# Kernel tuning notes

Hardware: AMD Instinct MI355X
Metric: run time of the kernel (lower is better)

Reference implementation:

```python
import jax, jax.numpy as jnp
import numpy as np

N_HEAD = 16
LN_EPS = 1e-5


def _ln(x, w, b):
    # torch LayerNorm computed in float32 then cast back (see LayerNorm.forward)
    xf = x.astype(jnp.float32)
    mu = jnp.mean(xf, axis=-1, keepdims=True)
    var = jnp.mean(jnp.square(xf - mu), axis=-1, keepdims=True)
    return ((xf - mu) * jax.lax.rsqrt(var + LN_EPS) * w + b).astype(x.dtype)


def setup_inputs() -> dict:
    key = jax.random.key(0)
    ks = jax.random.split(key, 16)
    B, S, C = 4, 1500, 1024
    A = 256  # adapter_dim
    F = 4 * C
    s = 0.02
    return {
        "x": jax.random.normal(ks[0], (B, S, C), jnp.float32),
        "Wq": jax.random.normal(ks[1], (C, C), jnp.float32) * s,
        "bq": jnp.zeros((C,), jnp.float32),
        "Wk": jax.random.normal(ks[2], (C, C), jnp.float32) * s,
        "Wv": jax.random.normal(ks[3], (C, C), jnp.float32) * s,
        "bv": jnp.zeros((C,), jnp.float32),
        "Wo": jax.random.normal(ks[4], (C, C), jnp.float32) * s,
        "bo": jnp.zeros((C,), jnp.float32),
        "ln_attn_w": jnp.ones((C,), jnp.float32),
        "ln_attn_b": jnp.zeros((C,), jnp.float32),
        "W1": jax.random.normal(ks[5], (F, C), jnp.float32) * s,
        "b1": jnp.zeros((F,), jnp.float32),
        "W2": jax.random.normal(ks[6], (C, F), jnp.float32) * s,
        "b2": jnp.zeros((C,), jnp.float32),
        "ln_mlp_w": jnp.ones((C,), jnp.float32),
        "ln_mlp_b": jnp.zeros((C,), jnp.float32),
        "Wds": jax.random.normal(ks[7], (A, C), jnp.float32) * s,
        "bds": jnp.zeros((A,), jnp.float32),
        "Wus": jax.random.normal(ks[8], (C, A), jnp.float32) * s,
        "bus": jnp.zeros((C,), jnp.float32),
    }


def reference(x, Wq, bq, Wk, Wv, bv, Wo, bo, ln_attn_w, ln_attn_b,
              W1, b1, W2, b2, ln_mlp_w, ln_mlp_b, Wds, bds, Wus, bus):
    B, S, C = x.shape
    H = N_HEAD
    D = C // H
    scale = D ** -0.25  # applied to both q and k, per qkv_attention

    # --- self-attention ---
    h = _ln(x, ln_attn_w, ln_attn_b)
    q = (h @ Wq.T + bq).reshape(B, S, H, D) * scale
    k = (h @ Wk.T).reshape(B, S, H, D) * scale  # key has no bias
    v = (h @ Wv.T + bv).reshape(B, S, H, D)
    qk = jnp.einsum("bqhd,bkhd->bhqk", q, k).astype(jnp.float32)
    w = jax.nn.softmax(qk, axis=-1).astype(x.dtype)
    wv = jnp.einsum("bhqk,bkhd->bqhd", w, v).reshape(B, S, C)
    x = x + (wv @ Wo.T + bo)

    # --- MLP (exact GELU, as nn.GELU default) ---
    h = _ln(x, ln_mlp_w, ln_mlp_b)
    x = x + (jax.nn.gelu(h @ W1.T + b1, approximate=False) @ W2.T + b2)

    # --- bottleneck adapter: x + us(gelu(ds(x))) ---
    x = x + (jax.nn.gelu(x @ Wds.T + bds, approximate=False) @ Wus.T + bus)
    return x
```

## Files before the change

kernel.cpp:

```cpp
#include <hip/hip_runtime.h>
#include <hip/hip_bf16.h>
#include <math.h>

typedef __bf16 bf16;
typedef __bf16 bf16x8 __attribute__((ext_vector_type(8)));
typedef float  f32x4  __attribute__((ext_vector_type(4)));

__device__ __forceinline__ void load16_lds(const bf16* g, bf16* l) {
    __builtin_amdgcn_global_load_lds(
        (__attribute__((address_space(1))) void*)(g),
        (__attribute__((address_space(3))) void*)(l), 16, 0, 0);
}

__device__ __forceinline__ float gelu_f(float x) {
    float u = 1.5957691216057308f * (x + 0.044715f * x * x * x);
    float e = __expf(u);
    float th = 1.0f - 2.0f / (1.0f + e);
    return 0.5f * x * (1.0f + th);
}

struct ConvArgs {
    const float* src[19];
    bf16* dst[19];
    int n[19];
    int bstart[20];
};
__global__ __launch_bounds__(256) void convert_many(ConvArgs a) {
    int blk = blockIdx.x;
    int s = 0;
    while (blk >= a.bstart[s + 1]) s++;
    const float* src = a.src[s];
    bf16* dst = a.dst[s];
    int n = a.n[s];
    int i0 = (blk - a.bstart[s]) * 2048;
#pragma unroll
    for (int e = 0; e < 8; e++) {
        int i = i0 + threadIdx.x + e * 256;
        if (i < n) dst[i] = (bf16)src[i];
    }
}

__global__ void zero_kernel(bf16* dst, int n) {
    int i = blockIdx.x * blockDim.x + threadIdx.x;
    if (i < n) dst[i] = (bf16)0.0f;
}

template<class XT>
__global__ __launch_bounds__(256) void ln_kernel(
    const XT* __restrict__ X, const bf16* __restrict__ w,
    const bf16* __restrict__ b, bf16* __restrict__ out)
{
    const int C = 1024;
    const int row = blockIdx.x;
    const int tid = threadIdx.x;
    const XT* xr = X + (size_t)row * C;
    float x0 = (float)xr[tid * 4 + 0], x1 = (float)xr[tid * 4 + 1];
    float x2 = (float)xr[tid * 4 + 2], x3 = (float)xr[tid * 4 + 3];
    float s  = x0 + x1 + x2 + x3;
    float sq = x0*x0 + x1*x1 + x2*x2 + x3*x3;
#pragma unroll
    for (int off = 32; off >= 1; off >>= 1) {
        s  += __shfl_xor(s,  off, 64);
        sq += __shfl_xor(sq, off, 64);
    }
    __shared__ float red[8];
    int wave = tid >> 6;
    if ((tid & 63) == 0) { red[wave] = s; red[4 + wave] = sq; }
    __syncthreads();
    float ts = red[0] + red[1] + red[2] + red[3];
    float tq = red[4] + red[5] + red[6] + red[7];
    float mean = ts * (1.0f / C);
    float var  = tq * (1.0f / C) - mean * mean;
    float rstd = rsqrtf(var + 1e-5f);
    float w0 = (float)w[tid*4+0], w1 = (float)w[tid*4+1], w2 = (float)w[tid*4+2], w3 = (float)w[tid*4+3];
    float b0 = (float)b[tid*4+0], b1 = (float)b[tid*4+1], b2 = (float)b[tid*4+2], b3 = (float)b[tid*4+3];
    bf16* orow = out + (size_t)row * C + tid * 4;
    orow[0] = (bf16)((x0 - mean) * rstd * w0 + b0);
    orow[1] = (bf16)((x1 - mean) * rstd * w1 + b1);
    orow[2] = (bf16)((x2 - mean) * rstd * w2 + b2);
    orow[3] = (bf16)((x3 - mean) * rstd * w3 + b3);
}

template<int ACT, int OMODE, class RT, class OT>
__global__ __launch_bounds__(256) void gemm_kernel(
    const bf16* __restrict__ A, const bf16* __restrict__ W,
    const bf16* __restrict__ bias, const RT* __restrict__ resid,
    OT* __restrict__ out, bf16* __restrict__ out_k, bf16* __restrict__ out_v,
    int M, int N, int K, float scale, int gmT, int gnT, int mQ)
{
    const int lin = blockIdx.x;
    const int xcd = lin & 7;
    const int t_  = lin >> 3;
    const int mt_ = (xcd & 3) + 4 * (t_ % mQ);
    const int nt_ = (xcd >> 2) + 2 * (t_ / mQ);
    if (mt_ >= gmT || nt_ >= gnT) return;
    const int m0 = mt_ * 128;
    const int n0 = nt_ * 128;

    __shared__ __align__(16) bf16 As[2][16 * 512];
    __shared__ __align__(16) bf16 Bs[2][16 * 512];
    const int tid = threadIdx.x;
    const int wave = tid >> 6, lane = tid & 63;
    const int lane15 = lane & 15, quad = lane >> 4;
    const int wm0 = (wave >> 1) * 64;
    const int wn0 = (wave & 1) * 64;
    f32x4 acc[4][4] = {};

    int ra0 = m0 + (2 * wave)     * 16 + lane15; if (ra0 > M - 1) ra0 = M - 1;
    int ra1 = m0 + (2 * wave + 1) * 16 + lane15; if (ra1 > M - 1) ra1 = M - 1;
    const int rb0 = n0 + (2 * wave)     * 16 + lane15;
    const int rb1 = n0 + (2 * wave + 1) * 16 + lane15;
    const bf16* a0 = A + (size_t)ra0 * K + quad * 8;
    const bf16* a1 = A + (size_t)ra1 * K + quad * 8;
    const bf16* w0 = W + (size_t)rb0 * K + quad * 8;
    const bf16* w1 = W + (size_t)rb1 * K + quad * 8;

    auto stage = [&](int buf, int k0) {
#pragma unroll
        for (int kk = 0; kk < 2; kk++) {
            load16_lds(a0 + k0 + kk * 32, &As[buf][((2 * wave)     * 2 + kk) * 512]);
            load16_lds(a1 + k0 + kk * 32, &As[buf][((2 * wave + 1) * 2 + kk) * 512]);
            load16_lds(w0 + k0 + kk * 32, &Bs[buf][((2 * wave)     * 2 + kk) * 512]);
            load16_lds(w1 + k0 + kk * 32, &Bs[buf][((2 * wave + 1) * 2 + kk) * 512]);
        }
    };

    stage(0, 0);
    asm volatile("s_waitcnt vmcnt(0)" ::: "memory");
    __builtin_amdgcn_s_barrier();
    __builtin_amdgcn_sched_barrier(0);

    const int nsteps = K >> 6;
    int cur = 0;
    for (int t = 0; t < nsteps; t++) {
        if (t + 1 < nsteps) stage(cur ^ 1, (t + 1) << 6);
#pragma unroll
        for (int kk = 0; kk < 2; kk++) {
            bf16x8 af[4], bfr[4];
#pragma unroll
            for (int tt = 0; tt < 4; tt++) {
                af[tt]  = *(const bf16x8*)(&As[cur][(((wm0 >> 4) + tt) * 2 + kk) * 512 + lane * 8]);
                bfr[tt] = *(const bf16x8*)(&Bs[cur][(((wn0 >> 4) + tt) * 2 + kk) * 512 + lane * 8]);
            }
#pragma unroll
            for (int mt = 0; mt < 4; mt++)
#pragma unroll
                for (int nt = 0; nt < 4; nt++)
                    acc[mt][nt] = __builtin_amdgcn_mfma_f32_16x16x32_bf16(
                        af[mt], bfr[nt], acc[mt][nt], 0, 0, 0);
        }
        if (t + 1 < nsteps) {
            asm volatile("s_waitcnt vmcnt(0)" ::: "memory");
            __builtin_amdgcn_s_barrier();
            __builtin_amdgcn_sched_barrier(0);
        }
        cur ^= 1;
    }

#pragma unroll
    for (int mt = 0; mt < 4; mt++) {
#pragma unroll
        for (int r = 0; r < 4; r++) {
            int gm = m0 + wm0 + mt * 16 + quad * 4 + r;
            if (gm >= M) continue;
#pragma unroll
            for (int nt = 0; nt < 4; nt++) {
                int gn = n0 + wn0 + nt * 16 + lane15;
                float v = acc[mt][nt][r];
                if (bias) v += (float)bias[gn];
                if (OMODE == 2) {
                    if (gn < 2048) {
                        v *= scale;
                        if (gn < 1024) v *= 1.4426950408889634f;
                    }
                } else v *= scale;
                if (ACT == 1) v = gelu_f(v);
                if (OMODE == 2) {
                    if (gn < 1024) {
                        ((bf16*)out)[(size_t)gm * 1024 + gn] = (bf16)v;
                    } else if (gn < 2048) {
                        out_k[(size_t)gm * 1024 + (gn - 1024)] = (bf16)v;
                    } else {
                        int gg = gn - 2048;
                        int bb = gm / 1500;
                        int ss = gm - bb * 1500;
                        int hh = gg >> 6, dd = gg & 63;
                        out_v[(((size_t)bb * 16 + hh) * 64 + dd) * 1536 + ss] = (bf16)v;
                    }
                } else {
                    if (resid) v += (float)resid[(size_t)gm * N + gn];
                    out[(size_t)gm * N + gn] = (OT)v;
                }
            }
        }
    }
}

__global__ __launch_bounds__(256) void flash_attn_kernel(
    const bf16* __restrict__ Q, const bf16* __restrict__ Km,
    const bf16* __restrict__ Vt, bf16* __restrict__ O)
{
    const int S = 1500, C = 1024, SP = 1536;
    const int LDP = 72;
    __shared__ __align__(16) bf16 Ks[2][8 * 512];
    __shared__ __align__(16) bf16 Vs[2][8 * 512];
    __shared__ __align__(16) bf16 Ps[4 * 16 * LDP];
    const int tid = threadIdx.x;
    const int wave = tid >> 6, lane = tid & 63;
    const int lane15 = lane & 15, quad = lane >> 4;
    const int bh = blockIdx.y;
    const int q0 = blockIdx.x * 64;
    const size_t headoff = (size_t)(bh >> 4) * S * C + (size_t)(bh & 15) * 64;
    const size_t vtoff   = (size_t)bh * 64 * SP;

    bf16x8 qf[2];
    int qr = q0 + wave * 16 + lane15; if (qr > S - 1) qr = S - 1;
    qf[0] = *(const bf16x8*)(Q + headoff + (size_t)qr * C + quad * 8);
    qf[1] = *(const bf16x8*)(Q + headoff + (size_t)qr * C + 32 + quad * 8);

    const bf16* vbase = Vt + vtoff + (size_t)(wave * 16 + lane15) * SP + quad * 8;

    auto stageKV = [&](int buf, int kt) {
        const int j0 = kt * 64;
        int kr = j0 + wave * 16 + lane15; if (kr > S - 1) kr = S - 1;
        const bf16* kbase = Km + headoff + (size_t)kr * C + quad * 8;
#pragma unroll
        for (int kk = 0; kk < 2; kk++) {
            load16_lds(kbase + kk * 32,      &Ks[buf][(wave * 2 + kk) * 512]);
            load16_lds(vbase + j0 + kk * 32, &Vs[buf][(wave * 2 + kk) * 512]);
        }
    };

    float m_run[4], l_part[4];
    f32x4 o_acc[4] = {};
#pragma unroll
    for (int r = 0; r < 4; r++) { m_run[r] = 4.0f; l_part[r] = 0.0f; }

    stageKV(0, 0);
    asm volatile("s_waitcnt vmcnt(0)" ::: "memory");
    __builtin_amdgcn_s_barrier();
    __builtin_amdgcn_sched_barrier(0);

    int cur = 0;
    for (int kt = 0; kt < 24; kt++) {
        if (kt + 1 < 24) stageKV(cur ^ 1, kt + 1);
        const int j0 = kt * 64;

        f32x4 s[4] = {};
#pragma unroll
        for (int kk = 0; kk < 2; kk++) {
#pragma unroll
            for (int nt = 0; nt < 4; nt++) {
                bf16x8 kf = *(const bf16x8*)(&Ks[cur][(nt * 2 + kk) * 512 + lane * 8]);
                s[nt] = __builtin_amdgcn_mfma_f32_16x16x32_bf16(qf[kk], kf, s[nt], 0, 0, 0);
            }
        }
        if (kt == 23) {
#pragma unroll
            for (int nt = 0; nt < 4; nt++) {
                if (j0 + nt * 16 + lane15 >= S) {
#pragma unroll
                    for (int r = 0; r < 4; r++) s[nt][r] = -1e30f;
                }
            }
        }

        float tm[4];
#pragma unroll
        for (int r = 0; r < 4; r++)
            tm[r] = fmaxf(fmaxf(s[0][r], s[1][r]), fmaxf(s[2][r], s[3][r]));
        bool rec = (tm[0] > m_run[0]) | (tm[1] > m_run[1]) |
                   (tm[2] > m_run[2]) | (tm[3] > m_run[3]);
        if (__any(rec)) {
#pragma unroll
            for (int r = 0; r < 4; r++) {
                float rm = tm[r];
#pragma unroll
                for (int off = 1; off < 16; off <<= 1) rm = fmaxf(rm, __shfl_xor(rm, off, 64));
                float mnew  = fmaxf(m_run[r], rm);
                float alpha = __builtin_amdgcn_exp2f(m_run[r] - mnew);
                m_run[r] = mnew;
                l_part[r] *= alpha;
#pragma unroll
                for (int dt = 0; dt < 4; dt++) o_acc[dt][r] *= alpha;
            }
        }

#pragma unroll
        for (int nt = 0; nt < 4; nt++) {
#pragma unroll
            for (int r = 0; r < 4; r++) {
                float p = __builtin_amdgcn_exp2f(s[nt][r] - m_run[r]);
                l_part[r] += p;
                Ps[wave * 16 * LDP + (quad * 4 + r) * LDP + nt * 16 + lane15] = (bf16)p;
            }
        }
        asm volatile("s_waitcnt lgkmcnt(0)" ::: "memory");
        __builtin_amdgcn_sched_barrier(0);
#pragma unroll
        for (int kk = 0; kk < 2; kk++) {
            bf16x8 pf = *(const bf16x8*)(&Ps[wave * 16 * LDP + lane15 * LDP + kk * 32 + quad * 8]);
#pragma unroll
            for (int dt = 0; dt < 4; dt++) {
                bf16x8 vf = *(const bf16x8*)(&Vs[cur][(dt * 2 + kk) * 512 + lane * 8]);
                o_acc[dt] = __builtin_amdgcn_mfma_f32_16x16x32_bf16(pf, vf, o_acc[dt], 0, 0, 0);
            }
        }
        if (kt + 1 < 24) {
            asm volatile("s_waitcnt vmcnt(0)" ::: "memory");
            __builtin_amdgcn_s_barrier();
            __builtin_amdgcn_sched_barrier(0);
        }
        cur ^= 1;
    }

    float l_inv[4];
#pragma unroll
    for (int r = 0; r < 4; r++) {
        float ls = l_part[r];
#pragma unroll
        for (int off = 1; off < 16; off <<= 1) ls += __shfl_xor(ls, off, 64);
        l_inv[r] = 1.0f / ls;
    }

#pragma unroll
    for (int dt = 0; dt < 4; dt++) {
#pragma unroll
        for (int r = 0; r < 4; r++) {
            int row = q0 + wave * 16 + quad * 4 + r;
            if (row < S) {
                float v = o_acc[dt][r] * l_inv[r];
                O[headoff + (size_t)row * C + dt * 16 + lane15] = (bf16)v;
            }
        }
    }
}

extern "C" void kernel_launch(void* const* d_in, const int* in_sizes, int n_in,
                              void* d_out, int out_size, void* d_ws, size_t ws_size,
                              hipStream_t stream) {
    float* out = (float*)d_out;
    const float* x_f32 = (const float*)d_in[0];
    const int M = 6000, Cc = 1024, F = 4096, Aa = 256;
    const size_t MC = (size_t)M * Cc;
    const size_t VT_ELEMS = (size_t)64 * 64 * 1536;
    bf16* ws = (bf16*)d_ws;

    bf16* h1   = ws;
    bf16* kbuf = ws + MC;
    bf16* Vt   = ws + 2 * MC;
    bf16* g    = ws + 2 * MC + VT_ELEMS;
    bf16* q    = (bf16*)d_out;
    bf16* wv   = h1;
    bf16* x1   = q;
    bf16* h2   = kbuf;
    bf16* x2   = Vt;
    bf16* aact = kbuf;

    size_t off = 2 * MC + VT_ELEMS + (size_t)M * F;
    bf16* Wqkv = ws + off; off += (size_t)3 * 1024 * 1024;
    bf16* bqkv = ws + off; off += 3072;
    bf16* sWo  = ws + off; off += (size_t)1024 * 1024;
    bf16* sbo  = ws + off; off += 1024;
    bf16* slnw = ws + off; off += 1024;
    bf16* slnb = ws + off; off += 1024;
    bf16* sW1  = ws + off; off += (size_t)4096 * 1024;
    bf16* sb1  = ws + off; off += 4096;
    bf16* sW2  = ws + off; off += (size_t)1024 * 4096;
    bf16* sb2  = ws + off; off += 1024;
    bf16* sln2w = ws + off; off += 1024;
    bf16* sln2b = ws + off; off += 1024;
    bf16* sWds = ws + off; off += (size_t)256 * 1024;
    bf16* sbds = ws + off; off += 256;
    bf16* sWus = ws + off; off += (size_t)1024 * 256;
    bf16* sbus = ws + off; off += 1024;

    ConvArgs ca;
    const int srcidx[19] = {1, 3, 4, 2, 5, 6, 7, 8, 9, 10, 11, 12, 13, 14, 15, 16, 17, 18, 19};
    bf16* dsts[19] = {Wqkv, Wqkv + 1048576, Wqkv + 2097152, bqkv, bqkv + 2048,
                      sWo, sbo, slnw, slnb, sW1, sb1, sW2, sb2, sln2w, sln2b,
                      sWds, sbds, sWus, sbus};
    int bacc = 0;
    for (int i = 0; i < 19; i++) {
        ca.src[i] = (const float*)d_in[srcidx[i]];
        ca.dst[i] = dsts[i];
        ca.n[i] = in_sizes[srcidx[i]];
        ca.bstart[i] = bacc;
        bacc += (ca.n[i] + 2047) / 2048;
    }
    ca.bstart[19] = bacc;

    dim3 blk(256);
    convert_many<<<bacc, blk, 0, stream>>>(ca);
    zero_kernel<<<4, blk, 0, stream>>>(bqkv + 1024, 1024);

    const float scale = 0.35355339059327373f;
    const int gmT = 47, mQ = 12;
    auto grid_for = [&](int gnT) { int nQ = (gnT + 1) >> 1; return dim3(8 * mQ * nQ); };

    ln_kernel<float><<<M, blk, 0, stream>>>(x_f32, slnw, slnb, h1);
    gemm_kernel<0, 2, bf16, bf16><<<grid_for(24), blk, 0, stream>>>(
        h1, Wqkv, bqkv, (const bf16*)nullptr, q, kbuf, Vt, M, 3072, Cc, scale, gmT, 24, mQ);
    dim3 ga(24, 64);
    flash_attn_kernel<<<ga, blk, 0, stream>>>(q, kbuf, Vt, wv);
    gemm_kernel<0, 0, float, bf16><<<grid_for(8), blk, 0, stream>>>(
        wv, sWo, sbo, x_f32, x1, nullptr, nullptr, M, Cc, Cc, 1.0f, gmT, 8, mQ);
    ln_kernel<bf16><<<M, blk, 0, stream>>>(x1, sln2w, sln2b, h2);
    gemm_kernel<1, 0, bf16, bf16><<<grid_for(32), blk, 0, stream>>>(
        h2, sW1, sb1, (const bf16*)nullptr, g, nullptr, nullptr, M, F, Cc, 1.0f, gmT, 32, mQ);
    gemm_kernel<0, 0, bf16, bf16><<<grid_for(8), blk, 0, stream>>>(
        g, sW2, sb2, x1, x2, nullptr, nullptr, M, Cc, F, 1.0f, gmT, 8, mQ);
    gemm_kernel<1, 0, bf16, bf16><<<grid_for(2), blk, 0, stream>>>(
        x2, sWds, sbds, (const bf16*)nullptr, aact, nullptr, nullptr, M, Aa, Cc, 1.0f, gmT, 2, mQ);
    gemm_kernel<0, 0, bf16, float><<<grid_for(8), blk, 0, stream>>>(
        aact, sWus, sbus, x2, out, nullptr, nullptr, M, Cc, Aa, 1.0f, gmT, 8, mQ);
}
```

Measured before the change: 806.1 us.

## Add 256x256-tile GEMM kernel with 512 threads for QKV and FC1

```diff
diff --git a/kernel.cpp b/kernel.cpp
--- a/kernel.cpp
+++ b/kernel.cpp
@@ -17,6 +17,38 @@
     float e = __expf(u);
     float th = 1.0f - 2.0f / (1.0f + e);
     return 0.5f * x * (1.0f + th);
+}
+
+template<int ACT, int OMODE, class RT, class OT>
+__device__ __forceinline__ void gemm_epilogue_elem(
+    float v, int gm, int gn, int M, int N, float scale,
+    const bf16* __restrict__ bias, const RT* __restrict__ resid,
+    OT* __restrict__ out, bf16* __restrict__ out_k, bf16* __restrict__ out_v)
+{
+    if (bias) v += (float)bias[gn];
+    if (OMODE == 2) {
+        if (gn < 2048) {
+            v *= scale;
+            if (gn < 1024) v *= 1.4426950408889634f;
+        }
+    } else v *= scale;
+    if (ACT == 1) v = gelu_f(v);
+    if (OMODE == 2) {
+        if (gn < 1024) {
+            ((bf16*)out)[(size_t)gm * 1024 + gn] = (bf16)v;
+        } else if (gn < 2048) {
+            out_k[(size_t)gm * 1024 + (gn - 1024)] = (bf16)v;
+        } else {
+            int gg = gn - 2048;
+            int bb = gm / 1500;
+            int ss = gm - bb * 1500;
+            int hh = gg >> 6, dd = gg & 63;
+            out_v[(((size_t)bb * 16 + hh) * 64 + dd) * 1536 + ss] = (bf16)v;
+        }
+    } else {
+        if (resid) v += (float)resid[(size_t)gm * N + gn];
+        out[(size_t)gm * N + gn] = (OT)v;
+    }
 }
 
 struct ConvArgs {
@@ -166,31 +198,101 @@
 #pragma unroll
             for (int nt = 0; nt < 4; nt++) {
                 int gn = n0 + wn0 + nt * 16 + lane15;
-                float v = acc[mt][nt][r];
-                if (bias) v += (float)bias[gn];
-                if (OMODE == 2) {
-                    if (gn < 2048) {
-                        v *= scale;
-                        if (gn < 1024) v *= 1.4426950408889634f;
-                    }
-                } else v *= scale;
-                if (ACT == 1) v = gelu_f(v);
-                if (OMODE == 2) {
-                    if (gn < 1024) {
-                        ((bf16*)out)[(size_t)gm * 1024 + gn] = (bf16)v;
-                    } else if (gn < 2048) {
-                        out_k[(size_t)gm * 1024 + (gn - 1024)] = (bf16)v;
-                    } else {
-                        int gg = gn - 2048;
-                        int bb = gm / 1500;
-                        int ss = gm - bb * 1500;
-                        int hh = gg >> 6, dd = gg & 63;
-                        out_v[(((size_t)bb * 16 + hh) * 64 + dd) * 1536 + ss] = (bf16)v;
-                    }
-                } else {
-                    if (resid) v += (float)resid[(size_t)gm * N + gn];
-                    out[(size_t)gm * N + gn] = (OT)v;
-                }
+                gemm_epilogue_elem<ACT, OMODE, RT, OT>(
+                    acc[mt][nt][r], gm, gn, M, N, scale, bias, resid, out, out_k, out_v);
+            }
+        }
+    }
+}
+
+template<int ACT, int OMODE, class RT, class OT>
+__global__ __launch_bounds__(512, 2) void gemm256_kernel(
+    const bf16* __restrict__ A, const bf16* __restrict__ W,
+    const bf16* __restrict__ bias, const RT* __restrict__ resid,
+    OT* __restrict__ out, bf16* __restrict__ out_k, bf16* __restrict__ out_v,
+    int M, int N, int K, float scale, int gmT, int gnT, int mQ)
+{
+    const int lin = blockIdx.x;
+    const int xcd = lin & 7;
+    const int t_  = lin >> 3;
+    const int mt_ = (xcd & 3) + 4 * (t_ % mQ);
+    const int nt_ = (xcd >> 2) + 2 * (t_ / mQ);
+    if (mt_ >= gmT || nt_ >= gnT) return;
+    const int m0 = mt_ * 256;
+    const int n0 = nt_ * 256;
+
+    __shared__ __align__(16) bf16 As[2][32 * 512];
+    __shared__ __align__(16) bf16 Bs[2][32 * 512];
+    const int tid = threadIdx.x;
+    const int wave = tid >> 6, lane = tid & 63;
+    const int lane15 = lane & 15, quad = lane >> 4;
+    const int wm0 = (wave >> 2) * 128;
+    const int wn0 = (wave & 3) * 64;
+    f32x4 acc[8][4] = {};
+
+    int ra0 = m0 + (2 * wave)     * 16 + lane15; if (ra0 > M - 1) ra0 = M - 1;
+    int ra1 = m0 + (2 * wave + 1) * 16 + lane15; if (ra1 > M - 1) ra1 = M - 1;
+    const int rb0 = n0 + (2 * wave)     * 16 + lane15;
+    const int rb1 = n0 + (2 * wave + 1) * 16 + lane15;
+    const bf16* a0 = A + (size_t)ra0 * K + quad * 8;
+    const bf16* a1 = A + (size_t)ra1 * K + quad * 8;
+    const bf16* w0 = W + (size_t)rb0 * K + quad * 8;
+    const bf16* w1 = W + (size_t)rb1 * K + quad * 8;
+
+    auto stage = [&](int buf, int k0) {
+#pragma unroll
+        for (int kk = 0; kk < 2; kk++) {
+            load16_lds(a0 + k0 + kk * 32, &As[buf][((2 * wave)     * 2 + kk) * 512]);
+            load16_lds(a1 + k0 + kk * 32, &As[buf][((2 * wave + 1) * 2 + kk) * 512]);
+            load16_lds(w0 + k0 + kk * 32, &Bs[buf][((2 * wave)     * 2 + kk) * 512]);
+            load16_lds(w1 + k0 + kk * 32, &Bs[buf][((2 * wave + 1) * 2 + kk) * 512]);
+        }
+    };
+
+    stage(0, 0);
+    asm volatile("s_waitcnt vmcnt(0)" ::: "memory");
+    __builtin_amdgcn_s_barrier();
+    __builtin_amdgcn_sched_barrier(0);
+
+    const int nsteps = K >> 6;
+    int cur = 0;
+    for (int t = 0; t < nsteps; t++) {
+        if (t + 1 < nsteps) stage(cur ^ 1, (t + 1) << 6);
+#pragma unroll
+        for (int kk = 0; kk < 2; kk++) {
+            bf16x8 af[8], bfr[4];
+#pragma unroll
+            for (int tt = 0; tt < 8; tt++)
+                af[tt]  = *(const bf16x8*)(&As[cur][(((wm0 >> 4) + tt) * 2 + kk) * 512 + lane * 8]);
+#pragma unroll
+            for (int tt = 0; tt < 4; tt++)
+                bfr[tt] = *(const bf16x8*)(&Bs[cur][(((wn0 >> 4) + tt) * 2 + kk) * 512 + lane * 8]);
+#pragma unroll
+            for (int mt = 0; mt < 8; mt++)
+#pragma unroll
+                for (int nt = 0; nt < 4; nt++)
+                    acc[mt][nt] = __builtin_amdgcn_mfma_f32_16x16x32_bf16(
+                        af[mt], bfr[nt], acc[mt][nt], 0, 0, 0);
+        }
+        if (t + 1 < nsteps) {
+            asm volatile("s_waitcnt vmcnt(0)" ::: "memory");
+            __builtin_amdgcn_s_barrier();
+            __builtin_amdgcn_sched_barrier(0);
+        }
+        cur ^= 1;
+    }
+
+#pragma unroll
+    for (int mt = 0; mt < 8; mt++) {
+#pragma unroll
+        for (int r = 0; r < 4; r++) {
+            int gm = m0 + wm0 + mt * 16 + quad * 4 + r;
+            if (gm >= M) continue;
+#pragma unroll
+            for (int nt = 0; nt < 4; nt++) {
+                int gn = n0 + wn0 + nt * 16 + lane15;
+                gemm_epilogue_elem<ACT, OMODE, RT, OT>(
+                    acc[mt][nt][r], gm, gn, M, N, scale, bias, resid, out, out_k, out_v);
             }
         }
     }
@@ -391,23 +493,26 @@
     ca.bstart[19] = bacc;
 
     dim3 blk(256);
+    dim3 blk512(512);
     convert_many<<<bacc, blk, 0, stream>>>(ca);
     zero_kernel<<<4, blk, 0, stream>>>(bqkv + 1024, 1024);
 
     const float scale = 0.35355339059327373f;
     const int gmT = 47, mQ = 12;
     auto grid_for = [&](int gnT) { int nQ = (gnT + 1) >> 1; return dim3(8 * mQ * nQ); };
+    const int gmT2 = 24, mQ2 = 6;
+    auto grid256_for = [&](int gnT) { int nQ = (gnT + 1) >> 1; return dim3(8 * mQ2 * nQ); };
 
     ln_kernel<float><<<M, blk, 0, stream>>>(x_f32, slnw, slnb, h1);
-    gemm_kernel<0, 2, bf16, bf16><<<grid_for(24), blk, 0, stream>>>(
-        h1, Wqkv, bqkv, (const bf16*)nullptr, q, kbuf, Vt, M, 3072, Cc, scale, gmT, 24, mQ);
+    gemm256_kernel<0, 2, bf16, bf16><<<grid256_for(12), blk512, 0, stream>>>(
+        h1, Wqkv, bqkv, (const bf16*)nullptr, q, kbuf, Vt, M, 3072, Cc, scale, gmT2, 12, mQ2);
     dim3 ga(24, 64);
     flash_attn_kernel<<<ga, blk, 0, stream>>>(q, kbuf, Vt, wv);
     gemm_kernel<0, 0, float, bf16><<<grid_for(8), blk, 0, stream>>>(
         wv, sWo, sbo, x_f32, x1, nullptr, nullptr, M, Cc, Cc, 1.0f, gmT, 8, mQ);
     ln_kernel<bf16><<<M, blk, 0, stream>>>(x1, sln2w, sln2b, h2);
-    gemm_kernel<1, 0, bf16, bf16><<<grid_for(32), blk, 0, stream>>>(
-        h2, sW1, sb1, (const bf16*)nullptr, g, nullptr, nullptr, M, F, Cc, 1.0f, gmT, 32, mQ);
+    gemm256_kernel<1, 0, bf16, bf16><<<grid256_for(16), blk512, 0, stream>>>(
+        h2, sW1, sb1, (const bf16*)nullptr, g, nullptr, nullptr, M, F, Cc, 1.0f, gmT2, 16, mQ2);
     gemm_kernel<0, 0, bf16, bf16><<<grid_for(8), blk, 0, stream>>>(
         g, sW2, sb2, x1, x2, nullptr, nullptr, M, Cc, F, 1.0f, gmT, 8, mQ);
     gemm_kernel<1, 0, bf16, bf16><<<grid_for(2), blk, 0, stream>>>(
```

Measured after the change: 849.1 us. +5.3%, slower.

## Split-K the W2 and adapter down-projection GEMMs and drop LDS double buffering

Applied to the files above, without the earlier changes.

```diff
diff --git a/kernel.cpp b/kernel.cpp
--- a/kernel.cpp
+++ b/kernel.cpp
@@ -43,6 +43,30 @@
 __global__ void zero_kernel(bf16* dst, int n) {
     int i = blockIdx.x * blockDim.x + threadIdx.x;
     if (i < n) dst[i] = (bf16)0.0f;
+}
+
+template<int ACT, int RES>
+__global__ __launch_bounds__(256) void reduce_kernel(
+    const bf16* __restrict__ P0, const bf16* __restrict__ P1,
+    const bf16* __restrict__ bias, const bf16* __restrict__ resid,
+    bf16* __restrict__ out, int nmask, int total)
+{
+    int i = (blockIdx.x * 256 + threadIdx.x) * 8;
+    if (i >= total) return;
+    bf16x8 p0 = *(const bf16x8*)(P0 + i);
+    bf16x8 p1 = *(const bf16x8*)(P1 + i);
+    bf16x8 bb = *(const bf16x8*)(bias + (i & nmask));
+    bf16x8 rr;
+    if (RES) rr = *(const bf16x8*)(resid + i);
+    bf16x8 o;
+#pragma unroll
+    for (int j = 0; j < 8; j++) {
+        float v = (float)p0[j] + (float)p1[j] + (float)bb[j];
+        if (ACT) v = gelu_f(v);
+        if (RES) v += (float)rr[j];
+        o[j] = (bf16)v;
+    }
+    *(bf16x8*)(out + i) = o;
 }
 
 template<class XT>
@@ -86,7 +110,7 @@
     const bf16* __restrict__ A, const bf16* __restrict__ W,
     const bf16* __restrict__ bias, const RT* __restrict__ resid,
     OT* __restrict__ out, bf16* __restrict__ out_k, bf16* __restrict__ out_v,
-    int M, int N, int K, float scale, int gmT, int gnT, int mQ)
+    int M, int N, int K, float scale, int gmT, int gnT, int mQ, int ldK)
 {
     const int lin = blockIdx.x;
     const int xcd = lin & 7;
@@ -96,9 +120,11 @@
     if (mt_ >= gmT || nt_ >= gnT) return;
     const int m0 = mt_ * 128;
     const int n0 = nt_ * 128;
-
-    __shared__ __align__(16) bf16 As[2][16 * 512];
-    __shared__ __align__(16) bf16 Bs[2][16 * 512];
+    const int ksp = (OMODE == 3) ? blockIdx.y : 0;
+    const size_t ko = (size_t)ksp * K;
+
+    __shared__ __align__(16) bf16 As[16 * 512];
+    __shared__ __align__(16) bf16 Bs[16 * 512];
     const int tid = threadIdx.x;
     const int wave = tid >> 6, lane = tid & 63;
     const int lane15 = lane & 15, quad = lane >> 4;
@@ -110,37 +136,27 @@
     int ra1 = m0 + (2 * wave + 1) * 16 + lane15; if (ra1 > M - 1) ra1 = M - 1;
     const int rb0 = n0 + (2 * wave)     * 16 + lane15;
     const int rb1 = n0 + (2 * wave + 1) * 16 + lane15;
-    const bf16* a0 = A + (size_t)ra0 * K + quad * 8;
-    const bf16* a1 = A + (size_t)ra1 * K + quad * 8;
-    const bf16* w0 = W + (size_t)rb0 * K + quad * 8;
-    const bf16* w1 = W + (size_t)rb1 * K + quad * 8;
-
-    auto stage = [&](int buf, int k0) {
+    const bf16* a0 = A + (size_t)ra0 * ldK + ko + quad * 8;
+    const bf16* a1 = A + (size_t)ra1 * ldK + ko + quad * 8;
+    const bf16* w0 = W + (size_t)rb0 * ldK + ko + quad * 8;
+    const bf16* w1 = W + (size_t)rb1 * ldK + ko + quad * 8;
+
+    for (int k0 = 0; k0 < K; k0 += 64) {
 #pragma unroll
         for (int kk = 0; kk < 2; kk++) {
-            load16_lds(a0 + k0 + kk * 32, &As[buf][((2 * wave)     * 2 + kk) * 512]);
-            load16_lds(a1 + k0 + kk * 32, &As[buf][((2 * wave + 1) * 2 + kk) * 512]);
-            load16_lds(w0 + k0 + kk * 32, &Bs[buf][((2 * wave)     * 2 + kk) * 512]);
-            load16_lds(w1 + k0 + kk * 32, &Bs[buf][((2 * wave + 1) * 2 + kk) * 512]);
-        }
-    };
-
-    stage(0, 0);
-    asm volatile("s_waitcnt vmcnt(0)" ::: "memory");
-    __builtin_amdgcn_s_barrier();
-    __builtin_amdgcn_sched_barrier(0);
-
-    const int nsteps = K >> 6;
-    int cur = 0;
-    for (int t = 0; t < nsteps; t++) {
-        if (t + 1 < nsteps) stage(cur ^ 1, (t + 1) << 6);
+            load16_lds(a0 + k0 + kk * 32, &As[((2 * wave)     * 2 + kk) * 512]);
+            load16_lds(a1 + k0 + kk * 32, &As[((2 * wave + 1) * 2 + kk) * 512]);
+            load16_lds(w0 + k0 + kk * 32, &Bs[((2 * wave)     * 2 + kk) * 512]);
+            load16_lds(w1 + k0 + kk * 32, &Bs[((2 * wave + 1) * 2 + kk) * 512]);
+        }
+        __syncthreads();
 #pragma unroll
         for (int kk = 0; kk < 2; kk++) {
             bf16x8 af[4], bfr[4];
 #pragma unroll
             for (int tt = 0; tt < 4; tt++) {
-                af[tt]  = *(const bf16x8*)(&As[cur][(((wm0 >> 4) + tt) * 2 + kk) * 512 + lane * 8]);
-                bfr[tt] = *(const bf16x8*)(&Bs[cur][(((wn0 >> 4) + tt) * 2 + kk) * 512 + lane * 8]);
+                af[tt]  = *(const bf16x8*)(&As[(((wm0 >> 4) + tt) * 2 + kk) * 512 + lane * 8]);
+                bfr[tt] = *(const bf16x8*)(&Bs[(((wn0 >> 4) + tt) * 2 + kk) * 512 + lane * 8]);
             }
 #pragma unroll
             for (int mt = 0; mt < 4; mt++)
@@ -149,12 +165,7 @@
                     acc[mt][nt] = __builtin_amdgcn_mfma_f32_16x16x32_bf16(
                         af[mt], bfr[nt], acc[mt][nt], 0, 0, 0);
         }
-        if (t + 1 < nsteps) {
-            asm volatile("s_waitcnt vmcnt(0)" ::: "memory");
-            __builtin_amdgcn_s_barrier();
-            __builtin_amdgcn_sched_barrier(0);
-        }
-        cur ^= 1;
+        __syncthreads();
     }
 
 #pragma unroll
@@ -167,6 +178,11 @@
             for (int nt = 0; nt < 4; nt++) {
                 int gn = n0 + wn0 + nt * 16 + lane15;
                 float v = acc[mt][nt][r];
+                if (OMODE == 3) {
+                    bf16* po = ksp ? out_k : (bf16*)out;
+                    po[(size_t)gm * N + gn] = (bf16)v;
+                    continue;
+                }
                 if (bias) v += (float)bias[gn];
                 if (OMODE == 2) {
                     if (gn < 2048) {
@@ -356,6 +372,10 @@
     bf16* h2   = kbuf;
     bf16* x2   = Vt;
     bf16* aact = kbuf;
+    bf16* P0   = kbuf;
+    bf16* P1   = h1;
+    bf16* P0d  = h1;
+    bf16* P1d  = h1 + (size_t)M * Aa;
 
     size_t off = 2 * MC + VT_ELEMS + (size_t)M * F;
     bf16* Wqkv = ws + off; off += (size_t)3 * 1024 * 1024;
@@ -400,18 +420,33 @@
 
     ln_kernel<float><<<M, blk, 0, stream>>>(x_f32, slnw, slnb, h1);
     gemm_kernel<0, 2, bf16, bf16><<<grid_for(24), blk, 0, stream>>>(
-        h1, Wqkv, bqkv, (const bf16*)nullptr, q, kbuf, Vt, M, 3072, Cc, scale, gmT, 24, mQ);
+        h1, Wqkv, bqkv, (const bf16*)nullptr, q, kbuf, Vt, M, 3072, Cc, scale, gmT, 24, mQ, Cc);
     dim3 ga(24, 64);
     flash_attn_kernel<<<ga, blk, 0, stream>>>(q, kbuf, Vt, wv);
     gemm_kernel<0, 0, float, bf16><<<grid_for(8), blk, 0, stream>>>(
-        wv, sWo, sbo, x_f32, x1, nullptr, nullptr, M, Cc, Cc, 1.0f, gmT, 8, mQ);
+        wv, sWo, sbo, x_f32, x1, nullptr, nullptr, M, Cc, Cc, 1.0f, gmT, 8, mQ, Cc);
     ln_kernel<bf16><<<M, blk, 0, stream>>>(x1, sln2w, sln2b, h2);
     gemm_kernel<1, 0, bf16, bf16><<<grid_for(32), blk, 0, stream>>>(
-        h2, sW1, sb1, (const bf16*)nullptr, g, nullptr, nullptr, M, F, Cc, 1.0f, gmT, 32, mQ);
-    gemm_kernel<0, 0, bf16, bf16><<<grid_for(8), blk, 0, stream>>>(
-        g, sW2, sb2, x1, x2, nullptr, nullptr, M, Cc, F, 1.0f, gmT, 8, mQ);
-    gemm_kernel<1, 0, bf16, bf16><<<grid_for(2), blk, 0, stream>>>(
-        x2, sWds, sbds, (const bf16*)nullptr, aact, nullptr, nullptr, M, Aa, Cc, 1.0f, gmT, 2, mQ);
+        h2, sW1, sb1, (const bf16*)nullptr, g, nullptr, nullptr, M, F, Cc, 1.0f, gmT, 32, mQ, Cc);
+
+    {
+        dim3 gr = grid_for(8); gr.y = 2;
+        gemm_kernel<0, 3, bf16, bf16><<<gr, blk, 0, stream>>>(
+            g, sW2, nullptr, (const bf16*)nullptr, P0, P1, nullptr,
+            M, Cc, F / 2, 1.0f, gmT, 8, mQ, F);
+        reduce_kernel<0, 1><<<(M * Cc) / 2048, blk, 0, stream>>>(
+            P0, P1, sb2, x1, x2, Cc - 1, M * Cc);
+    }
+
+    {
+        dim3 gr = grid_for(2); gr.y = 2;
+        gemm_kernel<0, 3, bf16, bf16><<<gr, blk, 0, stream>>>(
+            x2, sWds, nullptr, (const bf16*)nullptr, P0d, P1d, nullptr,
+            M, Aa, Cc / 2, 1.0f, gmT, 2, mQ, Cc);
+        reduce_kernel<1, 0><<<(M * Aa) / 2048, blk, 0, stream>>>(
+            P0d, P1d, sbds, nullptr, aact, Aa - 1, M * Aa);
+    }
+
     gemm_kernel<0, 0, bf16, float><<<grid_for(8), blk, 0, stream>>>(
-        aact, sWus, sbus, x2, out, nullptr, nullptr, M, Cc, Aa, 1.0f, gmT, 8, mQ);
-}
+        aact, sWus, sbus, x2, out, nullptr, nullptr, M, Cc, Aa, 1.0f, gmT, 8, mQ, Aa);
+}
```

Measured after the change: 756.3 us. 1.07x faster.
